# Optimization experiments

Hardware: AMD Instinct MI355X
Metric: run time of the kernel (lower is better)

The kernel has to match this reference:

```python
import jax, jax.numpy as jnp
import numpy as np

B, S, H, DH = 2, 2048, 12, 64
D = H * DH          # dim_hidden = 768
DF = 4 * D          # dim_ffn = 3072
EPS = 1e-5


def layernorm(x, g, b):
    mu = jnp.mean(x, -1, keepdims=True)
    var = jnp.var(x, -1, keepdims=True)
    return (x - mu) * jax.lax.rsqrt(var + EPS) * g + b


def setup_inputs() -> dict:
    key = jax.random.key(0)
    ks = jax.random.split(key, 8)
    sc = 0.02
    x = jax.random.normal(ks[0], (B, S, D), jnp.float32)
    # causal mask: True where attention is NOT allowed (masked_fill semantics)
    causal = ~jnp.tril(jnp.ones((S, S), dtype=bool))
    attn_mask = jnp.broadcast_to(causal, (B, S, S))
    Wq = jax.random.normal(ks[1], (D, D), jnp.float32) * sc
    Wk = jax.random.normal(ks[2], (D, D), jnp.float32) * sc
    Wv = jax.random.normal(ks[3], (D, D), jnp.float32) * sc
    Wo = jax.random.normal(ks[4], (D, D), jnp.float32) * sc
    bo = jnp.zeros((D,), jnp.float32)
    g1 = jnp.ones((D,), jnp.float32)
    b1 = jnp.zeros((D,), jnp.float32)
    W1 = jax.random.normal(ks[5], (DF, D), jnp.float32) * sc  # conv1 (k=1) == linear
    bb1 = jnp.zeros((DF,), jnp.float32)
    W2 = jax.random.normal(ks[6], (D, DF), jnp.float32) * sc
    bb2 = jnp.zeros((D,), jnp.float32)
    g2 = jnp.ones((D,), jnp.float32)
    b2 = jnp.zeros((D,), jnp.float32)
    return dict(x=x, attn_mask=attn_mask, Wq=Wq, Wk=Wk, Wv=Wv, Wo=Wo, bo=bo,
                g1=g1, b1=b1, W1=W1, bb1=bb1, W2=W2, bb2=bb2, g2=g2, b2=b2)


def reference(x, attn_mask, Wq, Wk, Wv, Wo, bo, g1, b1, W1, bb1, W2, bb2, g2, b2):
    b, s, d = x.shape
    # projections and head split: (B, H, S, DH)
    q = (x @ Wq.T).reshape(b, s, H, DH).transpose(0, 2, 1, 3)
    k = (x @ Wk.T).reshape(b, s, H, DH).transpose(0, 2, 1, 3)
    v = (x @ Wv.T).reshape(b, s, H, DH).transpose(0, 2, 1, 3)
    scores = jnp.einsum('bhqd,bhkd->bhqk', q, k) / jnp.sqrt(jnp.float32(DH))
    scores = jnp.where(attn_mask[:, None, :, :], jnp.float32(-1e9), scores)
    attn_p = jax.nn.softmax(scores, axis=-1)          # (B, H, S, S)
    attn_v = jnp.einsum('bhqk,bhkd->bhqd', attn_p, v)
    attn_v = attn_v.transpose(0, 2, 1, 3).reshape(b, s, d)
    attn_out = attn_v @ Wo.T + bo
    h = layernorm(x + attn_out, g1, b1)
    f = jax.nn.gelu(h @ W1.T + bb1, approximate=False) @ W2.T + bb2
    y = layernorm(h + f, g2, b2)
    return y, attn_p
```

## Files before the change

### kernel.cpp

```cpp
#include <hip/hip_runtime.h>
#include <hip/hip_bf16.h>

#define DEV static __device__ __forceinline__

typedef short bf16x8  __attribute__((ext_vector_type(8)));
typedef short short4v __attribute__((ext_vector_type(4)));
typedef float f32x4   __attribute__((ext_vector_type(4)));

#define MFMA16(a,b,c) __builtin_amdgcn_mfma_f32_16x16x32_bf16((a),(b),(c),0,0,0)

#define BAR() __builtin_amdgcn_s_barrier()
#define WAITVM(N) asm volatile("s_waitcnt vmcnt(" #N ")" ::: "memory")

DEV short f2b(float f) {
  unsigned u = __float_as_uint(f);
  unsigned r = (u + 0x7fffu + ((u >> 16) & 1u)) >> 16;
  return (short)r;
}

DEV void gld16(const void* g, void* l) {
  __builtin_amdgcn_global_load_lds(
      (const __attribute__((address_space(1))) unsigned int*)g,
      (__attribute__((address_space(3))) unsigned int*)l, 16, 0, 0);
}

DEV bf16x8 ldfrag(const short* tile, int row, int unit) {
  return *(const bf16x8*)(tile + row * 64 + (((unit) ^ (row & 7)) << 3));
}

__global__ __launch_bounds__(256) void cast4(const float4* __restrict__ in,
                                             short4v* __restrict__ out, int n4) {
  int i = blockIdx.x * 256 + threadIdx.x;
  if (i < n4) {
    float4 v = in[i];
    short4v o;
    o[0] = f2b(v.x); o[1] = f2b(v.y); o[2] = f2b(v.z); o[3] = f2b(v.w);
    out[i] = o;
  }
}

__global__ __launch_bounds__(256) void cast4_m(
    const float4* __restrict__ s0, const float4* __restrict__ s1,
    const float4* __restrict__ s2, const float4* __restrict__ s3,
    short4v* __restrict__ d0, short4v* __restrict__ d1,
    short4v* __restrict__ d2, short4v* __restrict__ d3, int n4) {
  int i = blockIdx.x * 256 + threadIdx.x;
  if (i >= n4) return;
  int b = blockIdx.y;
  const float4* s = (b == 0) ? s0 : (b == 1) ? s1 : (b == 2) ? s2 : s3;
  short4v* d = (b == 0) ? d0 : (b == 1) ? d1 : (b == 2) ? d2 : d3;
  float4 v = s[i];
  short4v o;
  o[0] = f2b(v.x); o[1] = f2b(v.y); o[2] = f2b(v.z); o[3] = f2b(v.w);
  d[i] = o;
}

template <int MODE>
__global__ __launch_bounds__(256) void gemm_nt(
    const short* __restrict__ A, const short* __restrict__ Bw,
    float* __restrict__ outF, short* __restrict__ outB,
    short* __restrict__ outB2, short* __restrict__ outB3,
    const float* __restrict__ bias, int M, int N, int K, int Kstride,
    float scale) {
  __shared__ __align__(16) short As[2][128 * 64];
  __shared__ __align__(16) short Bs[2][128 * 64];
  int tid = threadIdx.x;
  int w = tid >> 6, lane = tid & 63, quad = lane >> 4, l15 = lane & 15;
  int m0 = blockIdx.x * 128, n0 = blockIdx.y * 128;
  int kbase = blockIdx.z * K;
  const short* Ap = A + kbase;
  const short* Bp = Bw + kbase;
  int wm = (w & 1) * 64, wn = (w >> 1) * 64;
  f32x4 acc[4][4] = {};

  auto stage = [&](int buf, int k0) {
#pragma unroll
    for (int i = 0; i < 4; i++) {
      int id = i * 256 + tid;
      int r = id >> 3, u = id & 7;
      int su = u ^ (r & 7);
      gld16(Ap + (size_t)(m0 + r) * Kstride + k0 + su * 8, &As[buf][id * 8]);
      gld16(Bp + (size_t)(n0 + r) * Kstride + k0 + su * 8, &Bs[buf][id * 8]);
    }
  };

  stage(0, 0);
  int cur = 0;
  for (int k0 = 0; k0 < K; k0 += 64) {
    if (k0 + 64 < K) { stage(cur ^ 1, k0 + 64); WAITVM(8); }
    else             { WAITVM(0); }
    BAR();
    const short* as = As[cur];
    const short* bs = Bs[cur];
#pragma unroll
    for (int kk = 0; kk < 2; kk++) {
      bf16x8 af[4], bfr[4];
#pragma unroll
      for (int mt = 0; mt < 4; mt++)
        af[mt] = ldfrag(as, wm + mt * 16 + l15, kk * 4 + quad);
#pragma unroll
      for (int nt = 0; nt < 4; nt++)
        bfr[nt] = ldfrag(bs, wn + nt * 16 + l15, kk * 4 + quad);
#pragma unroll
      for (int mt = 0; mt < 4; mt++)
#pragma unroll
        for (int nt = 0; nt < 4; nt++)
          acc[mt][nt] = MFMA16(af[mt], bfr[nt], acc[mt][nt]);
    }
    BAR();
    cur ^= 1;
  }

  if (MODE == 0) outF += (size_t)blockIdx.z * M * N;

#pragma unroll
  for (int mt = 0; mt < 4; mt++) {
#pragma unroll
    for (int nt = 0; nt < 4; nt++) {
      if (MODE == 4 && n0 >= 1536) {
        int gcol = n0 + wn + nt * 16 + l15;
        int col = gcol - 1536;
        int h_ = col >> 6, d_ = col & 63;
        int srow = m0 + wm + mt * 16 + quad * 4;
        int b_ = srow >> 11, s_ = srow & 2047;
        short4v pk;
#pragma unroll
        for (int reg = 0; reg < 4; reg++) pk[reg] = f2b(acc[mt][nt][reg]);
        *(short4v*)(outB3 + ((size_t)(b_ * 12 + h_) * 64 + d_) * 2048 + s_) = pk;
      } else {
#pragma unroll
        for (int reg = 0; reg < 4; reg++) {
          int grow = m0 + wm + mt * 16 + quad * 4 + reg;
          int gcol = n0 + wn + nt * 16 + l15;
          float v = acc[mt][nt][reg];
          if (MODE == 0) {
            outF[(size_t)grow * N + gcol] = v;
          } else if (MODE == 3) {
            float t = v + bias[gcol];
            float z = t * (1.0f + 0.044715f * t * t);
            float ge = t / (1.0f + __expf(-1.5957691216f * z));
            outB[(size_t)grow * N + gcol] = f2b(ge);
          } else if (MODE == 4) {
            int b_ = grow >> 11, s_ = grow & 2047;
            if (gcol < 768) {
              int h_ = gcol >> 6, d_ = gcol & 63;
              outB[(((size_t)(b_ * 12 + h_) << 11) + s_) * 64 + d_] = f2b(v * scale);
            } else {
              int col = gcol - 768;
              int h_ = col >> 6, d_ = col & 63;
              outB2[(((size_t)(b_ * 12 + h_) << 11) + s_) * 64 + d_] = f2b(v);
            }
          }
        }
      }
    }
  }
}

__global__ __launch_bounds__(256) void attn_kernel(
    const short* __restrict__ Qb, const short* __restrict__ Kb,
    const short* __restrict__ Vtb, float* __restrict__ Pout,
    short* __restrict__ Ov) {
  __shared__ __align__(16) short Qs[64 * 64];
  __shared__ __align__(16) short Ks[2][64 * 64];
  __shared__ __align__(16) short Vs[2][64 * 64];
  __shared__ __align__(16) short Ps[4 * 16 * 64];
  int tid = threadIdx.x, w = tid >> 6, lane = tid & 63;
  int quad = lane >> 4, l15 = lane & 15;
  int qb = (gridDim.x - 1) - blockIdx.x;
  int bh = blockIdx.y, q0 = qb << 6;
  const short* qp = Qb + ((size_t)bh << 17);
  const short* kp = Kb + ((size_t)bh << 17);
  const short* vp = Vtb + ((size_t)bh << 17);
  float* pp = Pout + ((size_t)bh << 22);

  auto stageK = [&](int buf, int kt) {
#pragma unroll
    for (int t = 0; t < 2; t++) {
      int row = t * 32 + w * 8 + (lane >> 3);
      int su = (lane & 7) ^ (row & 7);
      gld16(kp + ((size_t)((kt << 6) + row) << 6) + su * 8,
            &Ks[buf][row * 64 + (lane & 7) * 8]);
    }
  };
  auto stageV = [&](int buf, int kt) {
#pragma unroll
    for (int t = 0; t < 2; t++) {
      int row = t * 32 + w * 8 + (lane >> 3);
      int su = (lane & 7) ^ (row & 7);
      gld16(vp + (size_t)row * 2048 + (kt << 6) + su * 8,
            &Vs[buf][row * 64 + (lane & 7) * 8]);
    }
  };

#pragma unroll
  for (int t = 0; t < 2; t++) {
    int row = t * 32 + w * 8 + (lane >> 3);
    int su = (lane & 7) ^ (row & 7);
    gld16(qp + ((size_t)(q0 + row) << 6) + su * 8, Qs + row * 64 + (lane & 7) * 8);
  }
  stageK(0, 0);

  float lsum[4] = {0.f, 0.f, 0.f, 0.f};
  int cur = 0;

  for (int kt = 0; kt <= qb; kt++) {
    if (kt < qb) { stageK(cur ^ 1, kt + 1); WAITVM(2); }
    else         { WAITVM(0); }
    BAR();
    f32x4 sc[4] = {};
    int arow = w * 16 + l15;
    bf16x8 a0 = ldfrag(Qs, arow, quad), a1 = ldfrag(Qs, arow, 4 + quad);
    const short* ks = Ks[cur];
#pragma unroll
    for (int nt = 0; nt < 4; nt++) {
      int brow = nt * 16 + l15;
      bf16x8 b0 = ldfrag(ks, brow, quad), b1 = ldfrag(ks, brow, 4 + quad);
      sc[nt] = MFMA16(a0, b0, sc[nt]);
      sc[nt] = MFMA16(a1, b1, sc[nt]);
    }
    if (kt == qb) {
#pragma unroll
      for (int nt = 0; nt < 4; nt++) {
        int key = (kt << 6) + nt * 16 + l15;
#pragma unroll
        for (int reg = 0; reg < 4; reg++) {
          int qg = q0 + w * 16 + quad * 4 + reg;
          if (key > qg) sc[nt][reg] = -1e30f;
        }
      }
    }
#pragma unroll
    for (int reg = 0; reg < 4; reg++)
      lsum[reg] += __expf(sc[0][reg]) + __expf(sc[1][reg]) +
                   __expf(sc[2][reg]) + __expf(sc[3][reg]);
    BAR();
    cur ^= 1;
  }

  float rl[4];
#pragma unroll
  for (int reg = 0; reg < 4; reg++) {
    float s = lsum[reg];
#pragma unroll
    for (int xm = 1; xm < 16; xm <<= 1) s += __shfl_xor(s, xm, 64);
    rl[reg] = 1.0f / s;
  }
  f32x4 oacc[4] = {};

  stageK(cur, 0);
  stageV(cur, 0);
  for (int kt = 0; kt <= qb; kt++) {
    if (kt < qb) { stageK(cur ^ 1, kt + 1); stageV(cur ^ 1, kt + 1); WAITVM(4); }
    else         { WAITVM(0); }
    BAR();
    f32x4 sc[4] = {};
    int arow = w * 16 + l15;
    bf16x8 a0 = ldfrag(Qs, arow, quad), a1 = ldfrag(Qs, arow, 4 + quad);
    const short* ks = Ks[cur];
    const short* vs = Vs[cur];
#pragma unroll
    for (int nt = 0; nt < 4; nt++) {
      int brow = nt * 16 + l15;
      bf16x8 b0 = ldfrag(ks, brow, quad), b1 = ldfrag(ks, brow, 4 + quad);
      sc[nt] = MFMA16(a0, b0, sc[nt]);
      sc[nt] = MFMA16(a1, b1, sc[nt]);
    }
    if (kt == qb) {
#pragma unroll
      for (int nt = 0; nt < 4; nt++) {
        int key = (kt << 6) + nt * 16 + l15;
#pragma unroll
        for (int reg = 0; reg < 4; reg++) {
          int qg = q0 + w * 16 + quad * 4 + reg;
          if (key > qg) sc[nt][reg] = -1e30f;
        }
      }
    }
#pragma unroll
    for (int nt = 0; nt < 4; nt++) {
      int key = (kt << 6) + nt * 16 + l15;
#pragma unroll
      for (int reg = 0; reg < 4; reg++) {
        int qg = q0 + w * 16 + quad * 4 + reg;
        float p = __expf(sc[nt][reg]) * rl[reg];
        pp[((size_t)qg << 11) + key] = p;
        int prow = quad * 4 + reg, pcol = nt * 16 + l15;
        Ps[(w << 10) + prow * 64 + (((pcol >> 3) ^ (prow & 7)) << 3) + (pcol & 7)] =
            f2b(p);
      }
    }
    bf16x8 p0 = ldfrag(Ps + (w << 10), l15, quad);
    bf16x8 p1 = ldfrag(Ps + (w << 10), l15, 4 + quad);
#pragma unroll
    for (int dn = 0; dn < 4; dn++) {
      int vrow = dn * 16 + l15;
      bf16x8 v0 = ldfrag(vs, vrow, quad), v1 = ldfrag(vs, vrow, 4 + quad);
      oacc[dn] = MFMA16(p0, v0, oacc[dn]);
      oacc[dn] = MFMA16(p1, v1, oacc[dn]);
    }
    BAR();
    cur ^= 1;
  }

  int b_ = bh / 12, h_ = bh - b_ * 12;
#pragma unroll
  for (int dn = 0; dn < 4; dn++)
#pragma unroll
    for (int reg = 0; reg < 4; reg++) {
      int s_ = q0 + w * 16 + quad * 4 + reg;
      Ov[(size_t)((b_ << 11) + s_) * 768 + h_ * 64 + dn * 16 + l15] =
          f2b(oacc[dn][reg]);
    }

  int kstart = (qb + 1) << 6;
  if (kstart < 2048) {
    int nch = (2048 - kstart) >> 2;
    for (int r = 0; r < 64; r++) {
      float4* dst = (float4*)(pp + ((size_t)(q0 + r) << 11) + kstart);
      for (int c = tid; c < nch; c += 256) dst[c] = make_float4(0.f, 0.f, 0.f, 0.f);
    }
  }
}

template <int NP>
__global__ __launch_bounds__(256) void ln_fuse(
    const float* __restrict__ p0, const float* __restrict__ p1,
    const float* __restrict__ p2, const float* __restrict__ p3,
    const float* __restrict__ resid, const float* __restrict__ bias,
    const float* __restrict__ gw, const float* __restrict__ bw,
    float* __restrict__ outF, short* __restrict__ outB) {
  int row = blockIdx.x, tid = threadIdx.x;
  size_t off = (size_t)row * 768;
  float v[3];
#pragma unroll
  for (int i = 0; i < 3; i++) {
    int col = tid + i * 256;
    float t = p0[off + col] + resid[off + col] + bias[col];
    if (NP > 1) t += p1[off + col];
    if (NP > 2) t += p2[off + col];
    if (NP > 3) t += p3[off + col];
    v[i] = t;
  }
  float s = v[0] + v[1] + v[2];
  float ss = v[0] * v[0] + v[1] * v[1] + v[2] * v[2];
#pragma unroll
  for (int xm = 1; xm < 64; xm <<= 1) {
    s += __shfl_xor(s, xm, 64);
    ss += __shfl_xor(ss, xm, 64);
  }
  __shared__ float red[8];
  int w = tid >> 6, lane = tid & 63;
  if (lane == 0) { red[w] = s; red[w + 4] = ss; }
  __syncthreads();
  s = red[0] + red[1] + red[2] + red[3];
  ss = red[4] + red[5] + red[6] + red[7];
  float mu = s * (1.0f / 768.0f);
  float var = ss * (1.0f / 768.0f) - mu * mu;
  float inv = rsqrtf(var + 1e-5f);
  float* yF = outF + off;
#pragma unroll
  for (int i = 0; i < 3; i++) {
    int col = tid + i * 256;
    float y = (v[i] - mu) * inv * gw[col] + bw[col];
    yF[col] = y;
    if (outB) outB[off + col] = f2b(y);
  }
}

extern "C" void kernel_launch(void* const* d_in, const int* in_sizes, int n_in,
                              void* d_out, int out_size, void* d_ws, size_t ws_size,
                              hipStream_t stream) {
  const float* x  = (const float*)d_in[0];
  const float* Wq = (const float*)d_in[2];
  const float* Wk = (const float*)d_in[3];
  const float* Wv = (const float*)d_in[4];
  const float* Wo = (const float*)d_in[5];
  const float* bo = (const float*)d_in[6];
  const float* g1 = (const float*)d_in[7];
  const float* b1 = (const float*)d_in[8];
  const float* W1 = (const float*)d_in[9];
  const float* bb1 = (const float*)d_in[10];
  const float* W2 = (const float*)d_in[11];
  const float* bb2 = (const float*)d_in[12];
  const float* g2 = (const float*)d_in[13];
  const float* b2 = (const float*)d_in[14];

  const size_t P = (size_t)4096 * 768;

  char* cur = (char*)d_ws;
  auto take = [&](size_t n) { char* p = cur; cur += (n + 255) & ~(size_t)255; return p; };
  short* xb   = (short*)take(P * 2);
  short* wqkv = (short*)take((size_t)2304 * 768 * 2);
  short* wob  = (short*)take((size_t)589824 * 2);
  short* w1b  = (short*)take((size_t)2359296 * 2);
  short* w2b  = (short*)take((size_t)2359296 * 2);
  short* qbf  = (short*)take(P * 2);
  short* kbf  = (short*)take(P * 2);
  short* vtb  = (short*)take(P * 2);
  short* avb  = (short*)take(P * 2);
  short* hb   = (short*)take(P * 2);
  short* ub   = (short*)take((size_t)4096 * 3072 * 2);
  float* t1   = (float*)take(P * 2 * 4);
  float* hf   = (float*)take(P * 4);
  float* t2   = (float*)take(P * 4 * 4);

  float* y_out = (float*)d_out;
  float* p_out = (float*)d_out + P;

  cast4<<<3072, 256, 0, stream>>>((const float4*)x, (short4v*)xb, 786432);
  cast4_m<<<dim3(576, 4), 256, 0, stream>>>(
      (const float4*)Wq, (const float4*)Wk, (const float4*)Wv, (const float4*)Wo,
      (short4v*)wqkv, (short4v*)(wqkv + 589824), (short4v*)(wqkv + 1179648),
      (short4v*)wob, 147456);
  cast4_m<<<dim3(2304, 2), 256, 0, stream>>>(
      (const float4*)W1, (const float4*)W2, (const float4*)W1, (const float4*)W2,
      (short4v*)w1b, (short4v*)w2b, (short4v*)w1b, (short4v*)w2b, 589824);

  gemm_nt<4><<<dim3(32, 18), 256, 0, stream>>>(
      xb, wqkv, nullptr, qbf, kbf, vtb, nullptr, 4096, 2304, 768, 768, 0.125f);
  attn_kernel<<<dim3(32, 24), 256, 0, stream>>>(qbf, kbf, vtb, p_out, avb);
  gemm_nt<0><<<dim3(32, 6, 2), 256, 0, stream>>>(
      avb, wob, t1, nullptr, nullptr, nullptr, nullptr, 4096, 768, 384, 768, 1.0f);
  ln_fuse<2><<<4096, 256, 0, stream>>>(t1, t1 + P, nullptr, nullptr, x, bo,
                                       g1, b1, hf, hb);
  gemm_nt<3><<<dim3(32, 24), 256, 0, stream>>>(
      hb, w1b, nullptr, ub, nullptr, nullptr, bb1, 4096, 3072, 768, 768, 1.0f);
  gemm_nt<0><<<dim3(32, 6, 4), 256, 0, stream>>>(
      ub, w2b, t2, nullptr, nullptr, nullptr, nullptr, 4096, 768, 768, 3072, 1.0f);
  ln_fuse<4><<<4096, 256, 0, stream>>>(t2, t2 + P, t2 + 2 * P, t2 + 3 * P, hf, bb2,
                                       g2, b2, y_out, nullptr);
}
```

Before: 695.8 us.

## Fuse softmax row-sum pass into PV pass and normalize P afterwards

```diff
diff --git a/kernel.cpp b/kernel.cpp
--- a/kernel.cpp
+++ b/kernel.cpp
@@ -165,6 +165,7 @@
   __shared__ __align__(16) short Ks[2][64 * 64];
   __shared__ __align__(16) short Vs[2][64 * 64];
   __shared__ __align__(16) short Ps[4 * 16 * 64];
+  __shared__ float rowscale[64];
   int tid = threadIdx.x, w = tid >> 6, lane = tid & 63;
   int quad = lane >> 4, l15 = lane & 15;
   int qb = (gridDim.x - 1) - blockIdx.x;
@@ -200,56 +201,12 @@
     gld16(qp + ((size_t)(q0 + row) << 6) + su * 8, Qs + row * 64 + (lane & 7) * 8);
   }
   stageK(0, 0);
+  stageV(0, 0);
 
   float lsum[4] = {0.f, 0.f, 0.f, 0.f};
+  f32x4 oacc[4] = {};
   int cur = 0;
 
-  for (int kt = 0; kt <= qb; kt++) {
-    if (kt < qb) { stageK(cur ^ 1, kt + 1); WAITVM(2); }
-    else         { WAITVM(0); }
-    BAR();
-    f32x4 sc[4] = {};
-    int arow = w * 16 + l15;
-    bf16x8 a0 = ldfrag(Qs, arow, quad), a1 = ldfrag(Qs, arow, 4 + quad);
-    const short* ks = Ks[cur];
-#pragma unroll
-    for (int nt = 0; nt < 4; nt++) {
-      int brow = nt * 16 + l15;
-      bf16x8 b0 = ldfrag(ks, brow, quad), b1 = ldfrag(ks, brow, 4 + quad);
-      sc[nt] = MFMA16(a0, b0, sc[nt]);
-      sc[nt] = MFMA16(a1, b1, sc[nt]);
-    }
-    if (kt == qb) {
-#pragma unroll
-      for (int nt = 0; nt < 4; nt++) {
-        int key = (kt << 6) + nt * 16 + l15;
-#pragma unroll
-        for (int reg = 0; reg < 4; reg++) {
-          int qg = q0 + w * 16 + quad * 4 + reg;
-          if (key > qg) sc[nt][reg] = -1e30f;
-        }
-      }
-    }
-#pragma unroll
-    for (int reg = 0; reg < 4; reg++)
-      lsum[reg] += __expf(sc[0][reg]) + __expf(sc[1][reg]) +
-                   __expf(sc[2][reg]) + __expf(sc[3][reg]);
-    BAR();
-    cur ^= 1;
-  }
-
-  float rl[4];
-#pragma unroll
-  for (int reg = 0; reg < 4; reg++) {
-    float s = lsum[reg];
-#pragma unroll
-    for (int xm = 1; xm < 16; xm <<= 1) s += __shfl_xor(s, xm, 64);
-    rl[reg] = 1.0f / s;
-  }
-  f32x4 oacc[4] = {};
-
-  stageK(cur, 0);
-  stageV(cur, 0);
   for (int kt = 0; kt <= qb; kt++) {
     if (kt < qb) { stageK(cur ^ 1, kt + 1); stageV(cur ^ 1, kt + 1); WAITVM(4); }
     else         { WAITVM(0); }
@@ -283,11 +240,12 @@
 #pragma unroll
       for (int reg = 0; reg < 4; reg++) {
         int qg = q0 + w * 16 + quad * 4 + reg;
-        float p = __expf(sc[nt][reg]) * rl[reg];
-        pp[((size_t)qg << 11) + key] = p;
+        float e = __expf(sc[nt][reg]);
+        lsum[reg] += e;
+        pp[((size_t)qg << 11) + key] = e;
         int prow = quad * 4 + reg, pcol = nt * 16 + l15;
         Ps[(w << 10) + prow * 64 + (((pcol >> 3) ^ (prow & 7)) << 3) + (pcol & 7)] =
-            f2b(p);
+            f2b(e);
       }
     }
     bf16x8 p0 = ldfrag(Ps + (w << 10), l15, quad);
@@ -303,6 +261,16 @@
     cur ^= 1;
   }
 
+  float rl[4];
+#pragma unroll
+  for (int reg = 0; reg < 4; reg++) {
+    float s = lsum[reg];
+#pragma unroll
+    for (int xm = 1; xm < 16; xm <<= 1) s += __shfl_xor(s, xm, 64);
+    rl[reg] = 1.0f / s;
+    if (l15 == 0) rowscale[w * 16 + quad * 4 + reg] = rl[reg];
+  }
+
   int b_ = bh / 12, h_ = bh - b_ * 12;
 #pragma unroll
   for (int dn = 0; dn < 4; dn++)
@@ -310,8 +278,21 @@
     for (int reg = 0; reg < 4; reg++) {
       int s_ = q0 + w * 16 + quad * 4 + reg;
       Ov[(size_t)((b_ << 11) + s_) * 768 + h_ * 64 + dn * 16 + l15] =
-          f2b(oacc[dn][reg]);
-    }
+          f2b(oacc[dn][reg] * rl[reg]);
+    }
+
+  __syncthreads();
+
+  int kend4 = (qb + 1) << 4;
+  for (int r = 0; r < 64; r++) {
+    float scl = rowscale[r];
+    float4* rowp = (float4*)(pp + ((size_t)(q0 + r) << 11));
+    for (int c = tid; c < kend4; c += 256) {
+      float4 v = rowp[c];
+      v.x *= scl; v.y *= scl; v.z *= scl; v.w *= scl;
+      rowp[c] = v;
+    }
+  }
 
   int kstart = (qb + 1) << 6;
   if (kstart < 2048) {
```

New measurement: 810.1 us. 1.16x slower.
